# Optimization experiments

Hardware: AMD Instinct MI355X
Metric: run time of the kernel (lower is better)

## Reference

```python
import jax, jax.numpy as jnp
import numpy as np

EPS = 0.001  # threshold below which terms are skipped, per original code

def setup_inputs() -> dict:
    key = jax.random.key(0)
    k1, k2 = jax.random.split(key)
    B, S = 4096, 8192
    predictions = jax.random.normal(k1, (B, S), dtype=jnp.float32)
    targets = jax.random.normal(k2, (B, S), dtype=jnp.float32)
    return {"predictions": predictions, "targets": targets}

def reference(predictions, targets):
    B, S = targets.shape
    denom = jnp.abs(predictions) + jnp.abs(targets)          # [B,S]
    mask = denom >= EPS                                       # skip tiny denominators
    safe_denom = jnp.where(mask, denom, 1.0)
    ratio = jnp.where(mask, jnp.abs(targets - predictions) / safe_denom, 0.0)
    per_batch = ratio.sum(axis=1) * (200.0 / S)               # [B]
    return per_batch.sum() / B
```

## Files before the change

kernel.cpp:

```cpp
#include <hip/hip_runtime.h>

#define SMAPE_EPS 0.001f

__global__ __launch_bounds__(256) void smape_partial_kernel(
    const float* __restrict__ pred,
    const float* __restrict__ targ,
    float* __restrict__ partial,
    long long n4,
    long long n)
{
    const float4* __restrict__ p4 = reinterpret_cast<const float4*>(pred);
    const float4* __restrict__ t4 = reinterpret_cast<const float4*>(targ);

    long long idx    = (long long)blockIdx.x * blockDim.x + threadIdx.x;
    long long stride = (long long)gridDim.x * blockDim.x;

    float acc = 0.0f;

    for (long long i = idx; i < n4; i += stride) {
        float4 a = p4[i];
        float4 b = t4[i];

        {
            float d = fabsf(a.x) + fabsf(b.x);
            float num = fabsf(b.x - a.x);
            acc += (d >= SMAPE_EPS) ? (num / d) : 0.0f;
        }
        {
            float d = fabsf(a.y) + fabsf(b.y);
            float num = fabsf(b.y - a.y);
            acc += (d >= SMAPE_EPS) ? (num / d) : 0.0f;
        }
        {
            float d = fabsf(a.z) + fabsf(b.z);
            float num = fabsf(b.z - a.z);
            acc += (d >= SMAPE_EPS) ? (num / d) : 0.0f;
        }
        {
            float d = fabsf(a.w) + fabsf(b.w);
            float num = fabsf(b.w - a.w);
            acc += (d >= SMAPE_EPS) ? (num / d) : 0.0f;
        }
    }

    if (blockIdx.x == 0 && threadIdx.x == 0) {
        for (long long i = n4 * 4; i < n; ++i) {
            float a = pred[i];
            float b = targ[i];
            float d = fabsf(a) + fabsf(b);
            float num = fabsf(b - a);
            acc += (d >= SMAPE_EPS) ? (num / d) : 0.0f;
        }
    }

    #pragma unroll
    for (int off = 32; off > 0; off >>= 1)
        acc += __shfl_down(acc, off, 64);

    __shared__ float warp_sums[4];
    int lane = threadIdx.x & 63;
    int wid  = threadIdx.x >> 6;
    if (lane == 0) warp_sums[wid] = acc;
    __syncthreads();

    if (threadIdx.x == 0) {
        float s = warp_sums[0] + warp_sums[1] + warp_sums[2] + warp_sums[3];
        partial[blockIdx.x] = s;
    }
}

__global__ __launch_bounds__(256) void smape_final_kernel(
    const float* __restrict__ partial,
    int nblocks,
    float* __restrict__ out,
    float scale)
{
    float acc = 0.0f;
    for (int i = threadIdx.x; i < nblocks; i += blockDim.x)
        acc += partial[i];

    #pragma unroll
    for (int off = 32; off > 0; off >>= 1)
        acc += __shfl_down(acc, off, 64);

    __shared__ float warp_sums[4];
    int lane = threadIdx.x & 63;
    int wid  = threadIdx.x >> 6;
    if (lane == 0) warp_sums[wid] = acc;
    __syncthreads();

    if (threadIdx.x == 0) {
        float s = warp_sums[0] + warp_sums[1] + warp_sums[2] + warp_sums[3];
        out[0] = s * scale;
    }
}

extern "C" void kernel_launch(void* const* d_in, const int* in_sizes, int n_in,
                              void* d_out, int out_size, void* d_ws, size_t ws_size,
                              hipStream_t stream) {
    const float* pred = (const float*)d_in[0];
    const float* targ = (const float*)d_in[1];
    float* out        = (float*)d_out;
    float* partial    = (float*)d_ws;

    long long n  = (long long)in_sizes[0];
    long long n4 = n / 4;

    const int threads = 256;
    const int nblocks = 2048;

    float scale = (float)(200.0 / (double)n);

    smape_partial_kernel<<<nblocks, threads, 0, stream>>>(pred, targ, partial, n4, n);
    smape_final_kernel<<<1, threads, 0, stream>>>(partial, nblocks, out, scale);
}
```

Measured before the change: 47.44 us.

## Fuse final reduction via last-block ticket and use fast reciprocal

Merges the two-kernel reduction into one kernel where the last block to finish, found through an atomic ticket counter, sums the per-block partials. It also replaces the IEEE division with the hardware reciprocal approximation and splits the work into a fixed-count unrolled loop with two accumulators. This removes a second kernel launch and shortens the division sequence, but adds a memset launch per call and slightly lower precision in each ratio.

Result: slower. 111.0 us (+133.9%).

```diff
diff --git a/kernel.cpp b/kernel.cpp
--- a/kernel.cpp
+++ b/kernel.cpp
@@ -1,46 +1,61 @@
 #include <hip/hip_runtime.h>
 
 #define SMAPE_EPS 0.001f
+#define NBLOCKS   2048
+#define THREADS   256
 
-__global__ __launch_bounds__(256) void smape_partial_kernel(
+__global__ __launch_bounds__(THREADS) void smape_fused_kernel(
     const float* __restrict__ pred,
     const float* __restrict__ targ,
+    float* __restrict__ out,
     float* __restrict__ partial,
+    unsigned int* __restrict__ ticket,
     long long n4,
-    long long n)
+    long long n,
+    float scale)
 {
     const float4* __restrict__ p4 = reinterpret_cast<const float4*>(pred);
     const float4* __restrict__ t4 = reinterpret_cast<const float4*>(targ);
 
-    long long idx    = (long long)blockIdx.x * blockDim.x + threadIdx.x;
-    long long stride = (long long)gridDim.x * blockDim.x;
+    const long long idx    = (long long)blockIdx.x * THREADS + threadIdx.x;
+    const long long stride = (long long)gridDim.x * THREADS;
 
-    float acc = 0.0f;
+    float acc0 = 0.0f, acc1 = 0.0f;
 
-    for (long long i = idx; i < n4; i += stride) {
+    const long long iters = n4 / stride;
+    #pragma unroll 2
+    for (long long k = 0; k < iters; ++k) {
+        const long long i = idx + k * stride;
         float4 a = p4[i];
         float4 b = t4[i];
 
-        {
-            float d = fabsf(a.x) + fabsf(b.x);
-            float num = fabsf(b.x - a.x);
-            acc += (d >= SMAPE_EPS) ? (num / d) : 0.0f;
-        }
-        {
-            float d = fabsf(a.y) + fabsf(b.y);
-            float num = fabsf(b.y - a.y);
-            acc += (d >= SMAPE_EPS) ? (num / d) : 0.0f;
-        }
-        {
-            float d = fabsf(a.z) + fabsf(b.z);
-            float num = fabsf(b.z - a.z);
-            acc += (d >= SMAPE_EPS) ? (num / d) : 0.0f;
-        }
-        {
-            float d = fabsf(a.w) + fabsf(b.w);
-            float num = fabsf(b.w - a.w);
-            acc += (d >= SMAPE_EPS) ? (num / d) : 0.0f;
-        }
+        float dx = fabsf(a.x) + fabsf(b.x);
+        float dy = fabsf(a.y) + fabsf(b.y);
+        float dz = fabsf(a.z) + fabsf(b.z);
+        float dw = fabsf(a.w) + fabsf(b.w);
+
+        float nx = fabsf(b.x - a.x) * __builtin_amdgcn_rcpf(dx);
+        float ny = fabsf(b.y - a.y) * __builtin_amdgcn_rcpf(dy);
+        float nz = fabsf(b.z - a.z) * __builtin_amdgcn_rcpf(dz);
+        float nw = fabsf(b.w - a.w) * __builtin_amdgcn_rcpf(dw);
+
+        acc0 += (dx >= SMAPE_EPS) ? nx : 0.0f;
+        acc1 += (dy >= SMAPE_EPS) ? ny : 0.0f;
+        acc0 += (dz >= SMAPE_EPS) ? nz : 0.0f;
+        acc1 += (dw >= SMAPE_EPS) ? nw : 0.0f;
+    }
+
+    for (long long i = idx + iters * stride; i < n4; i += stride) {
+        float4 a = p4[i];
+        float4 b = t4[i];
+        float dx = fabsf(a.x) + fabsf(b.x);
+        float dy = fabsf(a.y) + fabsf(b.y);
+        float dz = fabsf(a.z) + fabsf(b.z);
+        float dw = fabsf(a.w) + fabsf(b.w);
+        acc0 += (dx >= SMAPE_EPS) ? fabsf(b.x - a.x) * __builtin_amdgcn_rcpf(dx) : 0.0f;
+        acc1 += (dy >= SMAPE_EPS) ? fabsf(b.y - a.y) * __builtin_amdgcn_rcpf(dy) : 0.0f;
+        acc0 += (dz >= SMAPE_EPS) ? fabsf(b.z - a.z) * __builtin_amdgcn_rcpf(dz) : 0.0f;
+        acc1 += (dw >= SMAPE_EPS) ? fabsf(b.w - a.w) * __builtin_amdgcn_rcpf(dw) : 0.0f;
     }
 
     if (blockIdx.x == 0 && threadIdx.x == 0) {
@@ -48,50 +63,50 @@
             float a = pred[i];
             float b = targ[i];
             float d = fabsf(a) + fabsf(b);
-            float num = fabsf(b - a);
-            acc += (d >= SMAPE_EPS) ? (num / d) : 0.0f;
+            acc0 += (d >= SMAPE_EPS) ? fabsf(b - a) * __builtin_amdgcn_rcpf(d) : 0.0f;
         }
     }
+
+    float acc = acc0 + acc1;
 
     #pragma unroll
     for (int off = 32; off > 0; off >>= 1)
         acc += __shfl_down(acc, off, 64);
 
     __shared__ float warp_sums[4];
-    int lane = threadIdx.x & 63;
-    int wid  = threadIdx.x >> 6;
+    __shared__ bool  is_last;
+    const int lane = threadIdx.x & 63;
+    const int wid  = threadIdx.x >> 6;
     if (lane == 0) warp_sums[wid] = acc;
     __syncthreads();
 
     if (threadIdx.x == 0) {
         float s = warp_sums[0] + warp_sums[1] + warp_sums[2] + warp_sums[3];
         partial[blockIdx.x] = s;
+        unsigned int old = __hip_atomic_fetch_add(ticket, 1u,
+                                                  __ATOMIC_ACQ_REL,
+                                                  __HIP_MEMORY_SCOPE_AGENT);
+        is_last = (old == (unsigned int)(gridDim.x - 1));
     }
-}
-
-__global__ __launch_bounds__(256) void smape_final_kernel(
-    const float* __restrict__ partial,
-    int nblocks,
-    float* __restrict__ out,
-    float scale)
-{
-    float acc = 0.0f;
-    for (int i = threadIdx.x; i < nblocks; i += blockDim.x)
-        acc += partial[i];
-
-    #pragma unroll
-    for (int off = 32; off > 0; off >>= 1)
-        acc += __shfl_down(acc, off, 64);
-
-    __shared__ float warp_sums[4];
-    int lane = threadIdx.x & 63;
-    int wid  = threadIdx.x >> 6;
-    if (lane == 0) warp_sums[wid] = acc;
     __syncthreads();
 
-    if (threadIdx.x == 0) {
-        float s = warp_sums[0] + warp_sums[1] + warp_sums[2] + warp_sums[3];
-        out[0] = s * scale;
+    if (is_last) {
+        float facc = 0.0f;
+        for (int i = threadIdx.x; i < (int)gridDim.x; i += THREADS) {
+            facc += __hip_atomic_load(&partial[i], __ATOMIC_RELAXED,
+                                      __HIP_MEMORY_SCOPE_AGENT);
+        }
+        #pragma unroll
+        for (int off = 32; off > 0; off >>= 1)
+            facc += __shfl_down(facc, off, 64);
+
+        __shared__ float fin[4];
+        if (lane == 0) fin[wid] = facc;
+        __syncthreads();
+        if (threadIdx.x == 0) {
+            float total = fin[0] + fin[1] + fin[2] + fin[3];
+            out[0] = total * scale;
+        }
     }
 }
 
@@ -101,16 +116,17 @@
     const float* pred = (const float*)d_in[0];
     const float* targ = (const float*)d_in[1];
     float* out        = (float*)d_out;
-    float* partial    = (float*)d_ws;
+
+    float* partial       = (float*)d_ws;
+    unsigned int* ticket = (unsigned int*)((char*)d_ws + NBLOCKS * sizeof(float));
 
     long long n  = (long long)in_sizes[0];
     long long n4 = n / 4;
 
-    const int threads = 256;
-    const int nblocks = 2048;
-
     float scale = (float)(200.0 / (double)n);
 
-    smape_partial_kernel<<<nblocks, threads, 0, stream>>>(pred, targ, partial, n4, n);
-    smape_final_kernel<<<1, threads, 0, stream>>>(partial, nblocks, out, scale);
+    hipMemsetAsync(ticket, 0, sizeof(unsigned int), stream);
+
+    smape_fused_kernel<<<NBLOCKS, THREADS, 0, stream>>>(
+        pred, targ, out, partial, ticket, n4, n, scale);
 }
```
